# Optimization experiments

Hardware: AMD Instinct MI355X
Metric: run time of the kernel (lower is better)

The kernel has to match this reference:

```python
import jax, jax.numpy as jnp
import numpy as np

NUM_HEADS = 8


def setup_inputs() -> dict:
    key = jax.random.key(0)
    k1, k2, k3, k4 = jax.random.split(key, 4)
    E = 256
    seq = jax.random.normal(k1, (4, 256, E, 16, 16), dtype=jnp.float32)
    W_qkv = jax.random.normal(k2, (3 * E, E), dtype=jnp.float32) * (E ** -0.5)
    W_out = jax.random.normal(k3, (E, E), dtype=jnp.float32) * (E ** -0.5)
    b_out = jax.random.normal(k4, (E,), dtype=jnp.float32)
    return {"seq": seq, "W_qkv": W_qkv, "W_out": W_out, "b_out": b_out,
            "n_sub_x": 16, "n_sub_y": 16}


def reference(seq, W_qkv, W_out, b_out, n_sub_x, n_sub_y):
    # seq: [b, s, c, h, w] -- a sequence of functions (tokens on spatial grids)
    b, s, c, h, w = seq.shape
    H = NUM_HEADS
    d = c // H  # head_dim

    # pointwise QKV projection along the channel axis (no bias)
    qkv = jnp.einsum('oc,bscxy->bsoxy', W_qkv, seq)  # [b, s, 3c, h, w]
    # channel layout per einops: (num_heads, split=3, head_dim)
    qkv = qkv.reshape(b, s, H, 3, d, h, w)
    qkv = jnp.transpose(qkv, (3, 0, 2, 1, 4, 5, 6))  # [3, b, H, s, d, h, w]
    q, k, v = qkv[0], qkv[1], qkv[2]

    # func_attention: L2 inner product over head_dim and spatial dims
    scale = 1.0 / np.sqrt(d * h * w).astype(np.float32)
    scores = jnp.einsum('bhqdxy,bhkdxy->bhqk', q, k) * scale  # [b, H, s, s]
    attn = jax.nn.softmax(scores, axis=-1)
    sa = jnp.einsum('bhqk,bhkdxy->bhqdxy', attn, v)  # [b, H, s, d, h, w]

    # merge heads back to channel axis: 'b h s d ... -> b s (h d) ...'
    sa = jnp.transpose(sa, (0, 2, 1, 3, 4, 5)).reshape(b, s, c, h, w)

    # output projection (with bias) along channels
    out = jnp.einsum('oc,bscxy->bsoxy', W_out, sa)
    out = out + b_out[None, None, :, None, None]
    return out
```

## Files before the change

kernel.cpp:

```cpp
#include <hip/hip_runtime.h>
#include <stdint.h>


#define DI __device__ __forceinline__

typedef __attribute__((ext_vector_type(4))) float  f32x4;
typedef __attribute__((ext_vector_type(8))) short  s16x8;
typedef __attribute__((ext_vector_type(4))) short  s16x4;
typedef __attribute__((ext_vector_type(8))) __bf16 bf16x8;

DI unsigned short f2bf(float f) {
    unsigned int u = __builtin_bit_cast(unsigned int, f);
    u = (u + 0x7fffu + ((u >> 16) & 1u)) >> 16;
    return (unsigned short)u;
}
DI bf16x8 asbf(s16x8 v) { return __builtin_bit_cast(bf16x8, v); }
#define MFMA16(a, b, c) __builtin_amdgcn_mfma_f32_16x16x32_bf16((a), (b), (c), 0, 0, 0)

#define GLOAD16(g, l) __builtin_amdgcn_global_load_lds( \
    (const __attribute__((address_space(1))) unsigned int*)(g), \
    (__attribute__((address_space(3))) unsigned int*)(l), 16, 0, 0)


DI void sgk_loadA(const unsigned short* __restrict__ Asrc,
                  s16x8 af[4][8], int wm, int lg, int lr) {
#pragma unroll
    for (int m = 0; m < 4; m++)
#pragma unroll
        for (int kf = 0; kf < 8; kf++)
            af[m][kf] = *(const s16x8*)(Asrc + (size_t)(wm + m * 16 + lr) * 256
                                        + kf * 32 + lg * 8);
}

DI void sgk_stage(const unsigned short* src, size_t rstride,
                  unsigned short* lds, int tid) {
#pragma unroll
    for (int i = 0; i < 8; i++)
        GLOAD16(src + (size_t)(i * 8) * rstride, lds + ((i * 256 + tid) << 3));
}

DI void sgk_mfma(const unsigned short* __restrict__ Bl,
                 const s16x8 af[4][8], f32x4 acc[4][4], int lg, int lr) {
    const f32x4 z4 = {0.f, 0.f, 0.f, 0.f};
    {
        s16x8 bfv[4];
#pragma unroll
        for (int n = 0; n < 4; n++)
            bfv[n] = *(const s16x8*)&Bl[(n * 16 + lr) * 256 + ((lg ^ (lr & 7)) << 3)];
#pragma unroll
        for (int n = 0; n < 4; n++) {
            bf16x8 bv = asbf(bfv[n]);
#pragma unroll
            for (int m = 0; m < 4; m++)
                acc[m][n] = MFMA16(asbf(af[m][0]), bv, z4);
        }
    }
#pragma unroll
    for (int kf = 1; kf < 8; kf++) {
        s16x8 bfv[4];
#pragma unroll
        for (int n = 0; n < 4; n++)
            bfv[n] = *(const s16x8*)&Bl[(n * 16 + lr) * 256
                                        + (((kf * 4 + lg) ^ (lr & 7)) << 3)];
#pragma unroll
        for (int n = 0; n < 4; n++) {
            bf16x8 bv = asbf(bfv[n]);
#pragma unroll
            for (int m = 0; m < 4; m++)
                acc[m][n] = MFMA16(asbf(af[m][kf]), bv, acc[m][n]);
        }
    }
}

#define SGK_SETUP()                                           \
    const int tid = threadIdx.x, ln = tid & 63, w = tid >> 6; \
    const int wm = w * 64;                                    \
    const int lg = ln >> 4, lr = ln & 15;                     \
    const size_t swoff = (size_t)(((tid & 31) ^ ((tid >> 5) & 7)) * 8); \
    const size_t srow = (size_t)(tid >> 5);

__global__ __launch_bounds__(64) void k_prep(
    const float* __restrict__ Wqkv, const float* __restrict__ Wout,
    unsigned short* __restrict__ Wbf)
{
    int r = blockIdx.x, ln = threadIdx.x;
    if (r < 768) {
        int split = r >> 8, hd = r & 255;
        const float* src = Wqkv + (size_t)(((hd >> 5) * 96) + split * 32 + (hd & 31)) * 256;
        f32x4 v = *(const f32x4*)(src + ln * 4);
        s16x4 h = {(short)f2bf(v.x), (short)f2bf(v.y), (short)f2bf(v.z), (short)f2bf(v.w)};
        *(s16x4*)&Wbf[(size_t)r * 256 + ln * 4] = h;
    } else {
        int o = r - 768;
        const float* src = Wout + (size_t)o * 256;
        int cp0 = ln * 4;
        int hh = cp0 >> 5;
        unsigned short vals[4];
#pragma unroll
        for (int j = 0; j < 4; j++) {
            int jj = (cp0 + j) & 31;
            int dd = (jj >> 1) + ((jj & 1) << 4);
            vals[j] = f2bf(src[hh * 32 + dd]);
        }
        s16x4 h4 = {(short)vals[0], (short)vals[1], (short)vals[2], (short)vals[3]};
        *(s16x4*)&Wbf[(size_t)r * 256 + cp0] = h4;
    }
}

__global__ __launch_bounds__(256) void k_tr(
    const float* __restrict__ seq, unsigned short* __restrict__ seqT)
{
    const int bs = blockIdx.x, tid = threadIdx.x;
    __shared__ __align__(16) unsigned short T[64][264];
    const float* src = seq + (size_t)bs * 65536;
    unsigned short* dst = seqT + (size_t)bs * 65536;

    for (int co = 0; co < 256; co += 64) {
        {
            int r = tid >> 2, p0 = (tid & 3) * 64;
            const float* s = src + (size_t)(co + r) * 256 + p0;
#pragma unroll
            for (int i = 0; i < 8; i++) {
                f32x4 a = *(const f32x4*)(s + i * 8);
                f32x4 b = *(const f32x4*)(s + i * 8 + 4);
                s16x8 h = {(short)f2bf(a.x), (short)f2bf(a.y), (short)f2bf(a.z),
                           (short)f2bf(a.w), (short)f2bf(b.x), (short)f2bf(b.y),
                           (short)f2bf(b.z), (short)f2bf(b.w)};
                *(s16x8*)&T[r][p0 + i * 8] = h;
            }
        }
        __syncthreads();
        {
            unsigned short e[64];
#pragma unroll
            for (int c = 0; c < 64; c++) e[c] = T[c][tid];
            unsigned short* d = dst + (size_t)tid * 256 + co;
#pragma unroll
            for (int j = 0; j < 8; j++) {
                s16x8 v = {(short)e[j * 8 + 0], (short)e[j * 8 + 1],
                           (short)e[j * 8 + 2], (short)e[j * 8 + 3],
                           (short)e[j * 8 + 4], (short)e[j * 8 + 5],
                           (short)e[j * 8 + 6], (short)e[j * 8 + 7]};
                *(s16x8*)(d + j * 8) = v;
            }
        }
        __syncthreads();
    }
}

__global__ __launch_bounds__(256, 2) void k_qkT(
    const unsigned short* __restrict__ seqT, const unsigned short* __restrict__ Wbf,
    unsigned short* __restrict__ Qb, unsigned short* __restrict__ Kb)
{
    const int mt = blockIdx.x >> 8, g = blockIdx.x & 255;

    __shared__ __align__(16) unsigned short Bb[2][16384];

    SGK_SETUP();

    s16x8 af[4][8];
    sgk_loadA(Wbf + (size_t)mt * 65536, af, wm, lg, lr);

    const unsigned short* Bsrc = seqT + (size_t)g * 262144 + srow * 256 + swoff;
    unsigned short* const dstB = mt ? Kb : Qb;

    sgk_stage(Bsrc, 256, Bb[0], tid);
    __syncthreads();

    for (int t = 0; t < 16; t++) {
        if (t + 1 < 16)
            sgk_stage(Bsrc + (size_t)(t + 1) * 16384, 256, Bb[(t + 1) & 1], tid);
        f32x4 acc[4][4];
        sgk_mfma(Bb[t & 1], af, acc, lg, lr);
        __syncthreads();

        const int bs = g * 4 + (t >> 2);
        const int b = bs >> 8, s = bs & 255;
        const int pb = (t & 3) * 64;
#pragma unroll
        for (int m = 0; m < 4; m++) {
#pragma unroll
            for (int rr = 0; rr < 4; rr++) {
                int oo = wm + m * 16 + lg * 4 + rr;
                size_t base = ((size_t)((b * 8 + (oo >> 5)) * 256 + s)) * 8192
                            + (size_t)(oo & 31) * 256 + pb + lr * 4;
                s16x4 pk = {(short)f2bf(acc[m][0][rr]), (short)f2bf(acc[m][1][rr]),
                            (short)f2bf(acc[m][2][rr]), (short)f2bf(acc[m][3][rr])};
                *(s16x4*)(dstB + base) = pk;
            }
        }
    }
}

__global__ __launch_bounds__(256, 2) void k_vT(
    const unsigned short* __restrict__ seqT, const unsigned short* __restrict__ Wbf,
    unsigned short* __restrict__ Vt)
{
    const int b = blockIdx.x >> 7, pg = blockIdx.x & 127;

    __shared__ __align__(16) unsigned short Bb[2][16384];

    SGK_SETUP();

    s16x8 af[4][8];
    sgk_loadA(Wbf + 131072, af, wm, lg, lr);

    const unsigned short* Bsrc = seqT + ((size_t)b * 256 + srow) * 65536 + swoff;

#define VT_TILE(t) (Bsrc + (size_t)(pg * 2 + ((t) >> 2)) * 256 \
                         + (size_t)(((t) & 3) * 64) * 65536)

    sgk_stage(VT_TILE(0), 65536, Bb[0], tid);
    __syncthreads();

    for (int t = 0; t < 8; t++) {
        if (t + 1 < 8)
            sgk_stage(VT_TILE(t + 1), 65536, Bb[(t + 1) & 1], tid);
        f32x4 acc[4][4];
        sgk_mfma(Bb[t & 1], af, acc, lg, lr);
        __syncthreads();

        const int p = pg * 2 + (t >> 2);
        const int sb = (t & 3) * 64;
#pragma unroll
        for (int m = 0; m < 4; m++) {
#pragma unroll
            for (int rr = 0; rr < 4; rr++) {
                int o = wm + m * 16 + lg * 4 + rr;
                size_t base = (size_t)(b * 8 + (o >> 5)) * 2097152
                            + (size_t)(p * 32 + (o & 31)) * 256 + sb + lr;
#pragma unroll
                for (int n = 0; n < 4; n++)
                    Vt[base + n * 16] = f2bf(acc[m][n][rr]);
            }
        }
    }
#undef VT_TILE
}

__global__ __launch_bounds__(256, 2) void k_avT(
    const unsigned short* __restrict__ Pb, const unsigned short* __restrict__ Vt,
    unsigned short* __restrict__ SAT)
{
    const int bh = blockIdx.x >> 4, nsl = blockIdx.x & 15;
    const int b = bh >> 3, h = bh & 7;

    __shared__ __align__(16) unsigned short Bb[2][16384];

    SGK_SETUP();

    s16x8 af[4][8];
    sgk_loadA(Pb + (size_t)bh * 65536, af, wm, lg, lr);

    const unsigned short* Bsrc = Vt + (size_t)bh * 2097152
                               + (size_t)(nsl * 512) * 256 + srow * 256 + swoff;

    sgk_stage(Bsrc, 256, Bb[0], tid);
    __syncthreads();

    for (int t = 0; t < 8; t++) {
        if (t + 1 < 8)
            sgk_stage(Bsrc + (size_t)(t + 1) * 16384, 256, Bb[(t + 1) & 1], tid);
        f32x4 acc[4][4];
        sgk_mfma(Bb[t & 1], af, acc, lg, lr);
        __syncthreads();

        const int fb = nsl * 512 + t * 64;
        const int p0 = fb >> 5;
#pragma unroll
        for (int m = 0; m < 4; m++) {
#pragma unroll
            for (int rr = 0; rr < 4; rr++) {
                int q = wm + m * 16 + lg * 4 + rr;
                size_t base = (size_t)(b * 256 + q) * 65536
                            + (size_t)p0 * 256 + h * 32 + lr * 2;
                unsigned int v01 = (unsigned int)f2bf(acc[m][0][rr])
                                 | ((unsigned int)f2bf(acc[m][1][rr]) << 16);
                unsigned int v23 = (unsigned int)f2bf(acc[m][2][rr])
                                 | ((unsigned int)f2bf(acc[m][3][rr]) << 16);
                *(unsigned int*)(SAT + base) = v01;
                *(unsigned int*)(SAT + base + 256) = v23;
            }
        }
    }
}

__global__ __launch_bounds__(256, 2) void k_outT(
    const unsigned short* __restrict__ SAT, const unsigned short* __restrict__ Wbf,
    const float* __restrict__ bias, float* __restrict__ out)
{
    const int g = blockIdx.x;

    __shared__ __align__(16) unsigned short Bb[2][16384];

    SGK_SETUP();

    s16x8 af[4][8];
    sgk_loadA(Wbf + 196608, af, wm, lg, lr);

    float bo[4][4];
#pragma unroll
    for (int m = 0; m < 4; m++)
#pragma unroll
        for (int rr = 0; rr < 4; rr++)
            bo[m][rr] = bias[wm + m * 16 + lg * 4 + rr];

    const unsigned short* Bsrc = SAT + (size_t)g * 131072 + srow * 256 + swoff;

    sgk_stage(Bsrc, 256, Bb[0], tid);
    __syncthreads();

    for (int t = 0; t < 8; t++) {
        if (t + 1 < 8)
            sgk_stage(Bsrc + (size_t)(t + 1) * 16384, 256, Bb[(t + 1) & 1], tid);
        f32x4 acc[4][4];
        sgk_mfma(Bb[t & 1], af, acc, lg, lr);
        __syncthreads();

        const int bs = g * 2 + (t >> 2);
        const int pb = (t & 3) * 64;
#pragma unroll
        for (int m = 0; m < 4; m++) {
#pragma unroll
            for (int rr = 0; rr < 4; rr++) {
                int o = wm + m * 16 + lg * 4 + rr;
                float* d = out + ((size_t)bs * 256 + o) * 256 + pb + lr;
#pragma unroll
                for (int n = 0; n < 4; n++)
                    d[n * 16] = acc[m][n][rr] + bo[m][rr];
            }
        }
    }
}

DI void cls_stage(const unsigned short* gp, size_t stride,
                  unsigned short* lbase, int w) {
#pragma unroll
    for (int i = 0; i < 4; i++)
        GLOAD16(gp + (size_t)(i * 8) * stride, lbase + (w * 4 + i) * 512);
}

DI void cls_mfma(const unsigned short* __restrict__ Al,
                 const unsigned short* __restrict__ Bl,
                 f32x4 acc[4][4], int wm, int wn, int lg, int lr) {
#pragma unroll
    for (int kk = 0; kk < 2; kk++) {
        int off = (((kk * 4 + lg) ^ (lr & 7)) << 3);
        s16x8 af[4];
#pragma unroll
        for (int m = 0; m < 4; m++)
            af[m] = *(const s16x8*)&Al[(wm + m * 16 + lr) * 64 + off];
        s16x8 bf[4];
#pragma unroll
        for (int n = 0; n < 4; n++)
            bf[n] = *(const s16x8*)&Bl[(wn + n * 16 + lr) * 64 + off];
#pragma unroll
        for (int n = 0; n < 4; n++) {
            bf16x8 bv = asbf(bf[n]);
#pragma unroll
            for (int m = 0; m < 4; m++)
                acc[m][n] = MFMA16(asbf(af[m]), bv, acc[m][n]);
        }
    }
}

__global__ __launch_bounds__(256, 2) void k_scores(
    const unsigned short* __restrict__ Qb, const unsigned short* __restrict__ Kb,
    float* __restrict__ Sp)
{
    const int bh = blockIdx.y;
    const int kc = blockIdx.x & 3, st = (blockIdx.x >> 2) & 1, mt = blockIdx.x >> 3;
    const int tid = threadIdx.x, ln = tid & 63, w = tid >> 6;
    const int wm = (w >> 1) * 64, wn = (w & 1) * 64;
    const int lg = ln >> 4, lr = ln & 15;
    const int srow = ln >> 3;
    const int schk = (ln & 7) ^ srow;

    __shared__ __align__(16) unsigned short Ab[2][8192];
    __shared__ __align__(16) unsigned short Bb[2][8192];

    f32x4 acc[4][4];
    const f32x4 z4 = {0.f, 0.f, 0.f, 0.f};
#pragma unroll
    for (int m = 0; m < 4; m++)
#pragma unroll
        for (int n = 0; n < 4; n++) acc[m][n] = z4;

    const unsigned short* gA = Qb + (size_t)(bh * 256 + mt * 128 + w * 32 + srow) * 8192
                             + kc * 2048 + schk * 8;
    const unsigned short* gB = Kb + (size_t)(bh * 256 + st * 128 + w * 32 + srow) * 8192
                             + kc * 2048 + schk * 8;

    cls_stage(gA, 8192, Ab[0], w);
    cls_stage(gB, 8192, Bb[0], w);
    __syncthreads();
    for (int t = 0; t < 32; t++) {
        if (t + 1 < 32) {
            cls_stage(gA + (size_t)(t + 1) * 64, 8192, Ab[(t + 1) & 1], w);
            cls_stage(gB + (size_t)(t + 1) * 64, 8192, Bb[(t + 1) & 1], w);
        }
        cls_mfma(Ab[t & 1], Bb[t & 1], acc, wm, wn, lg, lr);
        __syncthreads();
    }

    float* dst = Sp + (size_t)kc * 2097152
               + (size_t)(bh * 256 + mt * 128 + wm) * 256 + st * 128 + wn;
#pragma unroll
    for (int m = 0; m < 4; m++) {
#pragma unroll
        for (int rr = 0; rr < 4; rr++) {
            float* d = dst + (size_t)(m * 16 + lg * 4 + rr) * 256 + lr;
#pragma unroll
            for (int n = 0; n < 4; n++)
                d[n * 16] = acc[m][n][rr];
        }
    }
}

__global__ __launch_bounds__(256) void k_softmax(
    const float* __restrict__ Sp, unsigned short* __restrict__ Pb)
{
    const int tid = threadIdx.x, ln = tid & 63;
    const int row = blockIdx.x * 4 + (tid >> 6);
    const float scale = 0.011048543456039806f;

    const float* p0 = Sp + (size_t)row * 256 + ln * 4;
    f32x4 v = *(const f32x4*)p0;
#pragma unroll
    for (int k = 1; k < 4; k++)
        v += *(const f32x4*)(p0 + (size_t)k * 2097152);
    v *= scale;

    float m = fmaxf(fmaxf(v.x, v.y), fmaxf(v.z, v.w));
#pragma unroll
    for (int off = 32; off; off >>= 1) m = fmaxf(m, __shfl_xor(m, off));
    float e0 = __expf(v.x - m), e1 = __expf(v.y - m);
    float e2 = __expf(v.z - m), e3 = __expf(v.w - m);
    float sum = e0 + e1 + e2 + e3;
#pragma unroll
    for (int off = 32; off; off >>= 1) sum += __shfl_xor(sum, off);
    float inv = 1.f / sum;
    s16x4 p = {(short)f2bf(e0 * inv), (short)f2bf(e1 * inv),
               (short)f2bf(e2 * inv), (short)f2bf(e3 * inv)};
    *(s16x4*)(Pb + (size_t)row * 256 + ln * 4) = p;
}

extern "C" void kernel_launch(void* const* d_in, const int* in_sizes, int n_in,
                              void* d_out, int out_size, void* d_ws, size_t ws_size,
                              hipStream_t stream)
{
    const float* seq  = (const float*)d_in[0];
    const float* Wqkv = (const float*)d_in[1];
    const float* Wout = (const float*)d_in[2];
    const float* bout = (const float*)d_in[3];

    unsigned short* Qb = (unsigned short*)d_out;
    unsigned short* Kb = Qb + 67108864;

    unsigned short* Vt   = (unsigned short*)d_ws;
    unsigned short* seqT = Vt + 67108864;
    float*          Sp   = (float*)seqT;
    unsigned short* SAT  = seqT;
    unsigned short* Pb   = (unsigned short*)d_ws + 134217728;
    unsigned short* Wbf  = Pb + 2097152;

    float* out = (float*)d_out;

    k_prep<<<dim3(1024), dim3(64), 0, stream>>>(Wqkv, Wout, Wbf);
    k_tr<<<dim3(1024), dim3(256), 0, stream>>>(seq, seqT);
    k_qkT<<<dim3(512), dim3(256), 0, stream>>>(seqT, Wbf, Qb, Kb);
    k_vT<<<dim3(512), dim3(256), 0, stream>>>(seqT, Wbf, Vt);
    k_scores<<<dim3(16, 32), dim3(256), 0, stream>>>(Qb, Kb, Sp);
    k_softmax<<<dim3(2048), dim3(256), 0, stream>>>(Sp, Pb);
    k_avT<<<dim3(512), dim3(256), 0, stream>>>(Pb, Vt, SAT);
    k_outT<<<dim3(512), dim3(256), 0, stream>>>(SAT, Wbf, bout, out);
}
```

Baseline: 538.2 us.

## Merge Q/K projection blocks, vectorize V stores, reorder scores grid, permute P layout

The Q and K projections now run in one 512-thread block that stages each seq tile once and shares it between Q and K waves, halving B-tile loads. The V projection switches from scalar bf16 stores to packed 4-element stores by permuting the key-position layout within 64-element groups. Softmax writes P in a matching permuted order so the AV product stays consistent. The scores grid is flattened and reordered so blocks sharing a row tile run close together. Risks include fewer blocks for QK and scattered scalar stores in softmax.

New measurement: 522.9 us. 1.03x faster.

```diff
diff --git a/kernel.cpp b/kernel.cpp
--- a/kernel.cpp
+++ b/kernel.cpp
@@ -37,6 +37,13 @@
 #pragma unroll
     for (int i = 0; i < 8; i++)
         GLOAD16(src + (size_t)(i * 8) * rstride, lds + ((i * 256 + tid) << 3));
+}
+
+DI void sgk_stage512(const unsigned short* src, size_t rstride,
+                     unsigned short* lds, int tid) {
+#pragma unroll
+    for (int i = 0; i < 4; i++)
+        GLOAD16(src + (size_t)(i * 16) * rstride, lds + ((i * 512 + tid) << 3));
 }
 
 DI void sgk_mfma(const unsigned short* __restrict__ Bl,
@@ -148,28 +155,28 @@
     }
 }
 
-__global__ __launch_bounds__(256, 2) void k_qkT(
+__global__ __launch_bounds__(512, 2) void k_qkT(
     const unsigned short* __restrict__ seqT, const unsigned short* __restrict__ Wbf,
     unsigned short* __restrict__ Qb, unsigned short* __restrict__ Kb)
 {
-    const int mt = blockIdx.x >> 8, g = blockIdx.x & 255;
+    const int g = blockIdx.x;
 
     __shared__ __align__(16) unsigned short Bb[2][16384];
 
     SGK_SETUP();
 
     s16x8 af[4][8];
-    sgk_loadA(Wbf + (size_t)mt * 65536, af, wm, lg, lr);
+    sgk_loadA(Wbf, af, wm, lg, lr);
 
     const unsigned short* Bsrc = seqT + (size_t)g * 262144 + srow * 256 + swoff;
-    unsigned short* const dstB = mt ? Kb : Qb;
-
-    sgk_stage(Bsrc, 256, Bb[0], tid);
+    unsigned short* const dstB = (w >= 4) ? Kb : Qb;
+
+    sgk_stage512(Bsrc, 256, Bb[0], tid);
     __syncthreads();
 
     for (int t = 0; t < 16; t++) {
         if (t + 1 < 16)
-            sgk_stage(Bsrc + (size_t)(t + 1) * 16384, 256, Bb[(t + 1) & 1], tid);
+            sgk_stage512(Bsrc + (size_t)(t + 1) * 16384, 256, Bb[(t + 1) & 1], tid);
         f32x4 acc[4][4];
         sgk_mfma(Bb[t & 1], af, acc, lg, lr);
         __syncthreads();
@@ -182,8 +189,9 @@
 #pragma unroll
             for (int rr = 0; rr < 4; rr++) {
                 int oo = wm + m * 16 + lg * 4 + rr;
-                size_t base = ((size_t)((b * 8 + (oo >> 5)) * 256 + s)) * 8192
-                            + (size_t)(oo & 31) * 256 + pb + lr * 4;
+                int o = oo & 255;
+                size_t base = ((size_t)((b * 8 + (o >> 5)) * 256 + s)) * 8192
+                            + (size_t)(o & 31) * 256 + pb + lr * 4;
                 s16x4 pk = {(short)f2bf(acc[m][0][rr]), (short)f2bf(acc[m][1][rr]),
                             (short)f2bf(acc[m][2][rr]), (short)f2bf(acc[m][3][rr])};
                 *(s16x4*)(dstB + base) = pk;
@@ -228,10 +236,10 @@
             for (int rr = 0; rr < 4; rr++) {
                 int o = wm + m * 16 + lg * 4 + rr;
                 size_t base = (size_t)(b * 8 + (o >> 5)) * 2097152
-                            + (size_t)(p * 32 + (o & 31)) * 256 + sb + lr;
-#pragma unroll
-                for (int n = 0; n < 4; n++)
-                    Vt[base + n * 16] = f2bf(acc[m][n][rr]);
+                            + (size_t)(p * 32 + (o & 31)) * 256 + sb + lr * 4;
+                s16x4 pk = {(short)f2bf(acc[m][0][rr]), (short)f2bf(acc[m][1][rr]),
+                            (short)f2bf(acc[m][2][rr]), (short)f2bf(acc[m][3][rr])};
+                *(s16x4*)(Vt + base) = pk;
             }
         }
     }
@@ -368,8 +376,10 @@
     const unsigned short* __restrict__ Qb, const unsigned short* __restrict__ Kb,
     float* __restrict__ Sp)
 {
-    const int bh = blockIdx.y;
-    const int kc = blockIdx.x & 3, st = (blockIdx.x >> 2) & 1, mt = blockIdx.x >> 3;
+    const int bid = blockIdx.x;
+    const int ms = bid >> 7, rem = bid & 127;
+    const int bh = rem >> 2, kc = rem & 3;
+    const int mt = ms >> 1, st = ms & 1;
     const int tid = threadIdx.x, ln = tid & 63, w = tid >> 6;
     const int wm = (w >> 1) * 64, wn = (w & 1) * 64;
     const int lg = ln >> 4, lr = ln & 15;
@@ -434,15 +444,22 @@
     float m = fmaxf(fmaxf(v.x, v.y), fmaxf(v.z, v.w));
 #pragma unroll
     for (int off = 32; off; off >>= 1) m = fmaxf(m, __shfl_xor(m, off));
-    float e0 = __expf(v.x - m), e1 = __expf(v.y - m);
-    float e2 = __expf(v.z - m), e3 = __expf(v.w - m);
-    float sum = e0 + e1 + e2 + e3;
+    float e[4];
+    e[0] = __expf(v.x - m); e[1] = __expf(v.y - m);
+    e[2] = __expf(v.z - m); e[3] = __expf(v.w - m);
+    float sum = e[0] + e[1] + e[2] + e[3];
 #pragma unroll
     for (int off = 32; off; off >>= 1) sum += __shfl_xor(sum, off);
     float inv = 1.f / sum;
-    s16x4 p = {(short)f2bf(e0 * inv), (short)f2bf(e1 * inv),
-               (short)f2bf(e2 * inv), (short)f2bf(e3 * inv)};
-    *(s16x4*)(Pb + (size_t)row * 256 + ln * 4) = p;
+
+    unsigned short* dst = Pb + (size_t)row * 256;
+#pragma unroll
+    for (int j = 0; j < 4; j++) {
+        int ks = ln * 4 + j;
+        int wv64 = ks & 63;
+        int pos = (ks & ~63) | (((wv64 & 15) << 2) + (wv64 >> 4));
+        dst[pos] = f2bf(e[j] * inv);
+    }
 }
 
 extern "C" void kernel_launch(void* const* d_in, const int* in_sizes, int n_in,
@@ -468,9 +485,9 @@
 
     k_prep<<<dim3(1024), dim3(64), 0, stream>>>(Wqkv, Wout, Wbf);
     k_tr<<<dim3(1024), dim3(256), 0, stream>>>(seq, seqT);
-    k_qkT<<<dim3(512), dim3(256), 0, stream>>>(seqT, Wbf, Qb, Kb);
+    k_qkT<<<dim3(256), dim3(512), 0, stream>>>(seqT, Wbf, Qb, Kb);
     k_vT<<<dim3(512), dim3(256), 0, stream>>>(seqT, Wbf, Vt);
-    k_scores<<<dim3(16, 32), dim3(256), 0, stream>>>(Qb, Kb, Sp);
+    k_scores<<<dim3(512), dim3(256), 0, stream>>>(Qb, Kb, Sp);
     k_softmax<<<dim3(2048), dim3(256), 0, stream>>>(Sp, Pb);
     k_avT<<<dim3(512), dim3(256), 0, stream>>>(Pb, Vt, SAT);
     k_outT<<<dim3(512), dim3(256), 0, stream>>>(SAT, Wbf, bout, out);
```
